# Kernel optimization log

Measured on AMD Instinct MI355X. Metric: run time of the kernel, lower is better.

## Reference

```python
import jax, jax.numpy as jnp
import numpy as np

B, S, D, H, HID = 8192, 16, 128, 8, 1024
DH = D // H  # 16
GCN, NUMF = 40, 103
EPS = 1e-5

def _make_pe():
    pos = np.arange(S, dtype=np.float64)[:, None]
    i = np.arange(D, dtype=np.float64)[None, :]
    pe = pos / np.power(10000.0, (i // 2 * 2.0) / D)
    pe[:, 0::2] = np.sin(pe[:, 0::2])
    pe[:, 1::2] = np.cos(pe[:, 1::2])
    return jnp.asarray(pe, dtype=jnp.float32)  # [S, D]

PE = _make_pe()

def setup_inputs() -> dict:
    key = jax.random.key(0)
    ks = jax.random.split(key, 16)
    rn = lambda k, shape, s=0.02: (jax.random.normal(k, shape, jnp.float32) * s)
    return {
        "x": jax.random.normal(ks[0], (B, S, D), jnp.float32),
        "gcn_i": jax.random.normal(ks[1], (B, GCN), jnp.float32),
        "num": jax.random.normal(ks[2], (B, NUMF), jnp.float32),
        # two independent encoder layers, params stacked on leading dim
        "Wq": rn(ks[3], (2, D, D)), "bq": jnp.zeros((2, D), jnp.float32),
        "Wk": rn(ks[4], (2, D, D)), "bk": jnp.zeros((2, D), jnp.float32),
        "Wv": rn(ks[5], (2, D, D)), "bv": jnp.zeros((2, D), jnp.float32),
        "Wo": rn(ks[6], (2, D, D)), "bo": jnp.zeros((2, D), jnp.float32),
        "ln1_g": jnp.ones((2, D), jnp.float32), "ln1_b": jnp.zeros((2, D), jnp.float32),
        "W1": rn(ks[7], (2, D, HID)), "b1": jnp.zeros((2, HID), jnp.float32),
        "W2": rn(ks[8], (2, HID, D)), "b2": jnp.zeros((2, D), jnp.float32),
        "ln2_g": jnp.ones((2, D), jnp.float32), "ln2_b": jnp.zeros((2, D), jnp.float32),
        # head
        "Wn": rn(ks[9], (NUMF, D)), "bnum": jnp.zeros((D,), jnp.float32),
        "bn_gamma": jnp.ones((D,), jnp.float32), "bn_beta": jnp.zeros((D,), jnp.float32),
        "Wf": rn(ks[10], (S * D + GCN + D, 1)), "bf": jnp.zeros((1,), jnp.float32),
    }

def _ln(x, g, b):
    m = x.mean(-1, keepdims=True)
    v = ((x - m) ** 2).mean(-1, keepdims=True)
    return (x - m) * jax.lax.rsqrt(v + EPS) * g + b

def reference(x, gcn_i, num, Wq, bq, Wk, bk, Wv, bv, Wo, bo, ln1_g, ln1_b,
              W1, b1, W2, b2, ln2_g, ln2_b, Wn, bnum, bn_gamma, bn_beta, Wf, bf):
    out = x + PE  # positional encoding (dropout = identity in eval)
    scale = DH ** -0.5
    for l in range(2):
        # NOTE: original uses a raw .view(B*H, -1, DH) (no transpose) -- faithful reshape
        q = (out @ Wq[l] + bq[l]).reshape(B * H, S, DH)
        k = (out @ Wk[l] + bk[l]).reshape(B * H, S, DH)
        v = (out @ Wv[l] + bv[l]).reshape(B * H, S, DH)
        attn = jax.nn.softmax(jnp.einsum('nsd,ntd->nst', q, k) * scale, axis=-1)
        ctx = jnp.einsum('nst,ntd->nsd', attn, v).reshape(B, S, D)
        h = _ln(ctx @ Wo[l] + bo[l] + out, ln1_g[l], ln1_b[l])
        ff = jax.nn.relu(h @ W1[l] + b1[l]) @ W2[l] + b2[l]
        out = _ln(ff + h, ln2_g[l], ln2_b[l])
    flat = out.reshape(B, S * D)  # [B, 2048]
    n = num @ Wn + bnum  # [B, 128]
    # BatchNorm1d, training-mode forward (biased batch variance)
    mu = n.mean(0)
    var = ((n - mu) ** 2).mean(0)
    n = (n - mu) * jax.lax.rsqrt(var + EPS) * bn_gamma + bn_beta
    p = jnp.concatenate([flat, gcn_i, n], axis=-1)  # [B, 2216]
    return jax.nn.sigmoid(p @ Wf + bf)
```

## Files before the change

### kernel.cpp

```cpp
#include <hip/hip_runtime.h>
#include <hip/hip_bf16.h>
#include <math.h>

#define B_SZ   8192
#define S_SZ   16
#define D_SZ   128
#define HID_SZ 1024
#define NUMF_SZ 103
#define GCN_SZ 40
#define G_B    4
#define NBLK   (B_SZ / G_B)
#define STRD   136

typedef short bh8 __attribute__((ext_vector_type(8)));
typedef float fx4 __attribute__((ext_vector_type(4)));

__device__ __forceinline__ fx4 mfma16(bh8 a, bh8 b, fx4 c) {
    return __builtin_amdgcn_mfma_f32_16x16x32_bf16(a, b, c, 0, 0, 0);
}

__device__ __forceinline__ unsigned short f2b(float f) {
    unsigned u = __float_as_uint(f);
    return (unsigned short)((u + 0x7fffu + ((u >> 16) & 1u)) >> 16);
}
__device__ __forceinline__ float bu2f(unsigned short u) {
    return __uint_as_float(((unsigned)u) << 16);
}

__global__ __launch_bounds__(256) void prep_weights(
    const float* __restrict__ Wq, const float* __restrict__ Wk,
    const float* __restrict__ Wv, const float* __restrict__ Wo,
    const float* __restrict__ W1, const float* __restrict__ W2,
    unsigned short* __restrict__ WswQ, unsigned short* __restrict__ WswK,
    unsigned short* __restrict__ WswV, unsigned short* __restrict__ WswO,
    unsigned short* __restrict__ Wsw1, unsigned short* __restrict__ Wsw2,
    float* __restrict__ PEt)
{
    int i = blockIdx.x * 256 + threadIdx.x;
    if (i < 2048) {
        int s = i >> 7, c = i & 127;
        float expo = (float)((c >> 1) * 2) * (1.0f / 128.0f);
        float denom = powf(10000.0f, expo);
        float ang = (float)s / denom;
        PEt[i] = (c & 1) ? cosf(ang) : sinf(ang);
    }
    if (i < 2 * 16384) {
        int l = i >> 14, r = i & 16383;
        int nt = r >> 11, ks = (r >> 9) & 3, lane = (r >> 3) & 63, e = r & 7;
        int k = ks * 32 + (lane >> 4) * 8 + e;
        int n = nt * 16 + (lane & 15);
        int s = l * 16384 + k * 128 + n;
        WswQ[i] = f2b(Wq[s]); WswK[i] = f2b(Wk[s]);
        WswV[i] = f2b(Wv[s]); WswO[i] = f2b(Wo[s]);
    }
    {
        int l = i >> 17, r = i & 131071;
        int nt = r >> 11, ks = (r >> 9) & 3, lane = (r >> 3) & 63, e = r & 7;
        int k = ks * 32 + (lane >> 4) * 8 + e;
        int n = nt * 16 + (lane & 15);
        Wsw1[i] = f2b(W1[l * 131072 + k * 1024 + n]);
    }
    {
        int l = i >> 17, r = i & 131071;
        int nt = r >> 14, kt = (r >> 9) & 31, lane = (r >> 3) & 63, e = r & 7;
        int k = kt * 32 + (lane >> 4) * 8 + e;
        int n = nt * 16 + (lane & 15);
        Wsw2[i] = f2b(W2[l * 131072 + k * 128 + n]);
    }
}

__global__ __launch_bounds__(256, 2) void encoder_fused(
    const float* __restrict__ x, const float* __restrict__ gcn,
    const float* __restrict__ bq, const float* __restrict__ bk,
    const float* __restrict__ bv, const float* __restrict__ bo,
    const float* __restrict__ ln1g, const float* __restrict__ ln1b,
    const float* __restrict__ b1, const float* __restrict__ b2p,
    const float* __restrict__ ln2g, const float* __restrict__ ln2b,
    const float* __restrict__ Wf,
    const unsigned short* __restrict__ WswQ, const unsigned short* __restrict__ WswK,
    const unsigned short* __restrict__ WswV, const unsigned short* __restrict__ WswO,
    const unsigned short* __restrict__ Wsw1, const unsigned short* __restrict__ Wsw2,
    const float* __restrict__ PEt,
    float* __restrict__ acc1)
{
    __shared__ unsigned short ACT[64][STRD];
    __shared__ unsigned short Qb[64][STRD];
    __shared__ unsigned short Kb[64][STRD];
    __shared__ unsigned short Vb[64][STRD];
    __shared__ float LNp[64][4][2];
    __shared__ float LNs[64][2];

    const int t = threadIdx.x;
    const int w = t >> 6, lane = t & 63;
    const int q = lane >> 4, ln = lane & 15;
    const int bbase = blockIdx.x * G_B;

    {
        const float4* xb = (const float4*)(x + (size_t)bbase * 2048);
        const float4* pe4 = (const float4*)PEt;
#pragma unroll
        for (int i = 0; i < 8; ++i) {
            int f4 = i * 256 + t;
            float4 xv = xb[f4];
            float4 pv = pe4[f4 & 511];
            int flat = f4 * 4;
            int row = flat >> 7, col = flat & 127;
            ushort4 pk = {f2b(xv.x + pv.x), f2b(xv.y + pv.y),
                          f2b(xv.z + pv.z), f2b(xv.w + pv.w)};
            *(ushort4*)&ACT[row][col] = pk;
        }
    }
    __syncthreads();

    for (int l = 0; l < 2; ++l) {
        {
            bh8 afr[4][4];
#pragma unroll
            for (int mt = 0; mt < 4; ++mt)
#pragma unroll
                for (int ks = 0; ks < 4; ++ks)
                    afr[mt][ks] = *(const bh8*)&ACT[mt * 16 + ln][ks * 32 + q * 8];
            const unsigned short* Wm[3] = {WswQ + l * 16384, WswK + l * 16384, WswV + l * 16384};
            const float* bias3[3] = {bq + l * 128, bk + l * 128, bv + l * 128};
#pragma unroll
            for (int mtx = 0; mtx < 3; ++mtx) {
                unsigned short (*dst)[STRD] = (mtx == 0) ? Qb : (mtx == 1) ? Kb : Vb;
#pragma unroll
                for (int i2 = 0; i2 < 2; ++i2) {
                    int nt = w * 2 + i2;
                    bh8 wfr[4];
#pragma unroll
                    for (int ks = 0; ks < 4; ++ks)
                        wfr[ks] = *(const bh8*)(Wm[mtx] + ((nt * 4 + ks) * 64 + lane) * 8);
                    int n = nt * 16 + ln;
                    float bb = bias3[mtx][n];
#pragma unroll
                    for (int mt = 0; mt < 4; ++mt) {
                        fx4 acc = {0.f, 0.f, 0.f, 0.f};
#pragma unroll
                        for (int ks = 0; ks < 4; ++ks) acc = mfma16(afr[mt][ks], wfr[ks], acc);
#pragma unroll
                        for (int r2 = 0; r2 < 4; ++r2)
                            dst[mt * 16 + q * 4 + r2][n] = f2b(acc[r2] + bb);
                    }
                }
            }
        }
        __syncthreads();

        {
            int base = w * 16;
            int g = lane >> 3, u0 = (lane & 7) * 2;
            float qr[2][16];
#pragma unroll
            for (int h = 0; h < 2; ++h) {
                int u = u0 + h;
                int qsr = base + 2 * g + (u >> 3), qc = (u & 7) * 16;
                bh8 a0 = *(const bh8*)&Qb[qsr][qc];
                bh8 a1 = *(const bh8*)&Qb[qsr][qc + 8];
#pragma unroll
                for (int e = 0; e < 8; ++e) {
                    qr[h][e] = bu2f((unsigned short)a0[e]);
                    qr[h][8 + e] = bu2f((unsigned short)a1[e]);
                }
            }
            float p[2][16];
#pragma unroll
            for (int tp = 0; tp < 16; ++tp) {
                int ksr = base + 2 * g + (tp >> 3), kc = (tp & 7) * 16;
                bh8 k0 = *(const bh8*)&Kb[ksr][kc];
                bh8 k1 = *(const bh8*)&Kb[ksr][kc + 8];
                float d0 = 0.f, d1 = 0.f;
#pragma unroll
                for (int e = 0; e < 8; ++e) {
                    float kv = bu2f((unsigned short)k0[e]);
                    d0 = fmaf(qr[0][e], kv, d0); d1 = fmaf(qr[1][e], kv, d1);
                }
#pragma unroll
                for (int e = 0; e < 8; ++e) {
                    float kv = bu2f((unsigned short)k1[e]);
                    d0 = fmaf(qr[0][8 + e], kv, d0); d1 = fmaf(qr[1][8 + e], kv, d1);
                }
                p[0][tp] = d0 * 0.25f; p[1][tp] = d1 * 0.25f;
            }
#pragma unroll
            for (int h = 0; h < 2; ++h) {
                float mx = -1e30f;
#pragma unroll
                for (int tp = 0; tp < 16; ++tp) mx = fmaxf(mx, p[h][tp]);
                float sum = 0.f;
#pragma unroll
                for (int tp = 0; tp < 16; ++tp) { p[h][tp] = __expf(p[h][tp] - mx); sum += p[h][tp]; }
                float is = 1.0f / sum;
#pragma unroll
                for (int tp = 0; tp < 16; ++tp) p[h][tp] *= is;
            }
            float ctx[2][16];
#pragma unroll
            for (int h = 0; h < 2; ++h)
#pragma unroll
                for (int e = 0; e < 16; ++e) ctx[h][e] = 0.f;
#pragma unroll
            for (int tp = 0; tp < 16; ++tp) {
                int vsr = base + 2 * g + (tp >> 3), vc = (tp & 7) * 16;
                bh8 v0 = *(const bh8*)&Vb[vsr][vc];
                bh8 v1 = *(const bh8*)&Vb[vsr][vc + 8];
#pragma unroll
                for (int e = 0; e < 8; ++e) {
                    float vv = bu2f((unsigned short)v0[e]);
                    ctx[0][e] = fmaf(p[0][tp], vv, ctx[0][e]);
                    ctx[1][e] = fmaf(p[1][tp], vv, ctx[1][e]);
                }
#pragma unroll
                for (int e = 0; e < 8; ++e) {
                    float vv = bu2f((unsigned short)v1[e]);
                    ctx[0][8 + e] = fmaf(p[0][tp], vv, ctx[0][8 + e]);
                    ctx[1][8 + e] = fmaf(p[1][tp], vv, ctx[1][8 + e]);
                }
            }
#pragma unroll
            for (int h = 0; h < 2; ++h) {
                int u = u0 + h;
                int s = base + 2 * g + (u >> 3), dc = (u & 7) * 16;
                bh8 c0, c1;
#pragma unroll
                for (int e = 0; e < 8; ++e) {
                    c0[e] = (short)f2b(ctx[h][e]);
                    c1[e] = (short)f2b(ctx[h][8 + e]);
                }
                *(bh8*)&Qb[s][dc] = c0;
                *(bh8*)&Qb[s][dc + 8] = c1;
            }
        }
        __syncthreads();

        fx4 Cv[2][4];
        {
            bh8 cfr[4][4];
#pragma unroll
            for (int mt = 0; mt < 4; ++mt)
#pragma unroll
                for (int ks = 0; ks < 4; ++ks)
                    cfr[mt][ks] = *(const bh8*)&Qb[mt * 16 + ln][ks * 32 + q * 8];
#pragma unroll
            for (int i2 = 0; i2 < 2; ++i2) {
                int nt = w * 2 + i2, n = nt * 16 + ln;
                bh8 wfr[4];
#pragma unroll
                for (int ks = 0; ks < 4; ++ks)
                    wfr[ks] = *(const bh8*)(WswO + l * 16384 + ((nt * 4 + ks) * 64 + lane) * 8);
                float bb = bo[l * 128 + n];
#pragma unroll
                for (int mt = 0; mt < 4; ++mt) {
                    fx4 acc = {0.f, 0.f, 0.f, 0.f};
#pragma unroll
                    for (int ks = 0; ks < 4; ++ks) acc = mfma16(cfr[mt][ks], wfr[ks], acc);
#pragma unroll
                    for (int r2 = 0; r2 < 4; ++r2)
                        Cv[i2][mt][r2] = acc[r2] + bb +
                            bu2f(ACT[mt * 16 + q * 4 + r2][n]);
                }
            }
        }
#pragma unroll
        for (int mt = 0; mt < 4; ++mt) {
            float s4[4], v4[4];
#pragma unroll
            for (int r2 = 0; r2 < 4; ++r2) {
                float a0 = Cv[0][mt][r2], a1 = Cv[1][mt][r2];
                float s = a0 + a1, v = a0 * a0 + a1 * a1;
#pragma unroll
                for (int m = 1; m < 16; m <<= 1) { s += __shfl_xor(s, m); v += __shfl_xor(v, m); }
                s4[r2] = s; v4[r2] = v;
            }
            if (ln < 8)
                LNp[mt * 16 + q * 4 + (ln >> 1)][w][ln & 1] = (ln & 1) ? v4[ln >> 1] : s4[ln >> 1];
        }
        __syncthreads();
        if (t < 64) {
            float s = LNp[t][0][0] + LNp[t][1][0] + LNp[t][2][0] + LNp[t][3][0];
            float v = LNp[t][0][1] + LNp[t][1][1] + LNp[t][2][1] + LNp[t][3][1];
            float mean = s * (1.0f / 128.0f);
            LNs[t][0] = mean;
            LNs[t][1] = rsqrtf(v * (1.0f / 128.0f) - mean * mean + 1e-5f);
        }
        __syncthreads();
#pragma unroll
        for (int i2 = 0; i2 < 2; ++i2) {
            int n = (w * 2 + i2) * 16 + ln;
            float gg = ln1g[l * 128 + n], be = ln1b[l * 128 + n];
#pragma unroll
            for (int mt = 0; mt < 4; ++mt)
#pragma unroll
                for (int r2 = 0; r2 < 4; ++r2) {
                    int row = mt * 16 + q * 4 + r2;
                    Kb[row][n] = f2b((Cv[i2][mt][r2] - LNs[row][0]) * LNs[row][1] * gg + be);
                }
        }
        __syncthreads();

        bh8 hfr[4][4];
#pragma unroll
        for (int mt = 0; mt < 4; ++mt)
#pragma unroll
            for (int ks = 0; ks < 4; ++ks)
                hfr[mt][ks] = *(const bh8*)&Kb[mt * 16 + ln][ks * 32 + q * 8];
        fx4 f2a[2][4];
#pragma unroll
        for (int i2 = 0; i2 < 2; ++i2)
#pragma unroll
            for (int mt = 0; mt < 4; ++mt) f2a[i2][mt] = fx4{0.f, 0.f, 0.f, 0.f};
        for (int ch = 0; ch < 8; ++ch) {
            bh8 w1fr[2][4];
#pragma unroll
            for (int i2 = 0; i2 < 2; ++i2) {
                int ntg = ch * 8 + w * 2 + i2;
#pragma unroll
                for (int ks = 0; ks < 4; ++ks)
                    w1fr[i2][ks] = *(const bh8*)(Wsw1 + l * 131072 + ((ntg * 4 + ks) * 64 + lane) * 8);
            }
#pragma unroll
            for (int mt = 0; mt < 4; ++mt) {
#pragma unroll
                for (int i2 = 0; i2 < 2; ++i2) {
                    fx4 acc = {0.f, 0.f, 0.f, 0.f};
#pragma unroll
                    for (int ks = 0; ks < 4; ++ks) acc = mfma16(hfr[mt][ks], w1fr[i2][ks], acc);
                    int nl = (w * 2 + i2) * 16 + ln;
                    float bb = b1[l * HID_SZ + ch * 128 + nl];
#pragma unroll
                    for (int r2 = 0; r2 < 4; ++r2) {
                        float vv = acc[r2] + bb;
                        Qb[mt * 16 + q * 4 + r2][nl] = f2b(vv > 0.f ? vv : 0.f);
                    }
                }
            }
            __syncthreads();
            bh8 w2fr[2][4];
#pragma unroll
            for (int i2 = 0; i2 < 2; ++i2)
#pragma unroll
                for (int ks = 0; ks < 4; ++ks)
                    w2fr[i2][ks] = *(const bh8*)(Wsw2 + l * 131072 +
                        (((w * 2 + i2) * 32 + ch * 4 + ks) * 64 + lane) * 8);
#pragma unroll
            for (int mt = 0; mt < 4; ++mt) {
                bh8 ffr[4];
#pragma unroll
                for (int ks = 0; ks < 4; ++ks)
                    ffr[ks] = *(const bh8*)&Qb[mt * 16 + ln][ks * 32 + q * 8];
#pragma unroll
                for (int i2 = 0; i2 < 2; ++i2)
#pragma unroll
                    for (int ks = 0; ks < 4; ++ks)
                        f2a[i2][mt] = mfma16(ffr[ks], w2fr[i2][ks], f2a[i2][mt]);
            }
            __syncthreads();
        }
        fx4 Cv2[2][4];
#pragma unroll
        for (int i2 = 0; i2 < 2; ++i2) {
            int n = (w * 2 + i2) * 16 + ln;
            float bb = b2p[l * 128 + n];
#pragma unroll
            for (int mt = 0; mt < 4; ++mt)
#pragma unroll
                for (int r2 = 0; r2 < 4; ++r2)
                    Cv2[i2][mt][r2] = f2a[i2][mt][r2] + bb +
                        bu2f(Kb[mt * 16 + q * 4 + r2][n]);
        }
#pragma unroll
        for (int mt = 0; mt < 4; ++mt) {
            float s4[4], v4[4];
#pragma unroll
            for (int r2 = 0; r2 < 4; ++r2) {
                float a0 = Cv2[0][mt][r2], a1 = Cv2[1][mt][r2];
                float s = a0 + a1, v = a0 * a0 + a1 * a1;
#pragma unroll
                for (int m = 1; m < 16; m <<= 1) { s += __shfl_xor(s, m); v += __shfl_xor(v, m); }
                s4[r2] = s; v4[r2] = v;
            }
            if (ln < 8)
                LNp[mt * 16 + q * 4 + (ln >> 1)][w][ln & 1] = (ln & 1) ? v4[ln >> 1] : s4[ln >> 1];
        }
        __syncthreads();
        if (t < 64) {
            float s = LNp[t][0][0] + LNp[t][1][0] + LNp[t][2][0] + LNp[t][3][0];
            float v = LNp[t][0][1] + LNp[t][1][1] + LNp[t][2][1] + LNp[t][3][1];
            float mean = s * (1.0f / 128.0f);
            LNs[t][0] = mean;
            LNs[t][1] = rsqrtf(v * (1.0f / 128.0f) - mean * mean + 1e-5f);
        }
        __syncthreads();
#pragma unroll
        for (int i2 = 0; i2 < 2; ++i2) {
            int n = (w * 2 + i2) * 16 + ln;
            float gg = ln2g[l * 128 + n], be = ln2b[l * 128 + n];
#pragma unroll
            for (int mt = 0; mt < 4; ++mt)
#pragma unroll
                for (int r2 = 0; r2 < 4; ++r2) {
                    int row = mt * 16 + q * 4 + r2;
                    ACT[row][n] = f2b((Cv2[i2][mt][r2] - LNs[row][0]) * LNs[row][1] * gg + be);
                }
        }
        __syncthreads();
    }

    {
        int bg = bbase + w;
        float part = 0.f;
        int srow = lane >> 2, c0 = (lane & 3) * 32;
#pragma unroll
        for (int i = 0; i < 4; ++i) {
            bh8 av = *(const bh8*)&ACT[w * 16 + srow][c0 + i * 8];
            int fl = srow * 128 + c0 + i * 8;
#pragma unroll
            for (int e = 0; e < 8; ++e)
                part = fmaf(bu2f((unsigned short)av[e]), Wf[fl + e], part);
        }
        if (lane < GCN_SZ)
            part = fmaf(gcn[(size_t)bg * GCN_SZ + lane], Wf[2048 + lane], part);
#pragma unroll
        for (int off = 32; off; off >>= 1) part += __shfl_xor(part, off);
        if (lane == 0) acc1[bg] = part;
    }
}

__global__ __launch_bounds__(256) void num_stats_kernel(
    const float* __restrict__ num, const float* __restrict__ Wn,
    const float* __restrict__ bnum,
    float* __restrict__ ssum, float* __restrict__ ssq)
{
    __shared__ float NUM[16][NUMF_SZ + 1];
    __shared__ float cred[4][128];
    const int t = threadIdx.x;
    const int b0 = blockIdx.x * 16;
    const int j = t & 127, sg = t >> 7, s0 = sg * 8;

    for (int idx = t; idx < 16 * NUMF_SZ; idx += 256) {
        int r = idx / NUMF_SZ, f = idx - r * NUMF_SZ;
        NUM[r][f] = num[(size_t)(b0 + r) * NUMF_SZ + f];
    }
    __syncthreads();

    float acc[8];
    float bnv = bnum[j];
#pragma unroll
    for (int r = 0; r < 8; ++r) acc[r] = bnv;
    for (int f = 0; f < NUMF_SZ; ++f) {
        float w = Wn[f * 128 + j];
#pragma unroll
        for (int r = 0; r < 8; ++r) acc[r] = fmaf(NUM[s0 + r][f], w, acc[r]);
    }
    float lsum = 0.f, lsq = 0.f;
#pragma unroll
    for (int r = 0; r < 8; ++r) {
        lsum += acc[r];
        lsq = fmaf(acc[r], acc[r], lsq);
    }
    cred[sg][j] = lsum;
    cred[2 + sg][j] = lsq;
    __syncthreads();
    if (sg == 0) atomicAdd(&ssum[j], cred[0][j] + cred[1][j]);
    else         atomicAdd(&ssq[j],  cred[2][j] + cred[3][j]);
}

__global__ __launch_bounds__(128) void final_kernel(
    const float* __restrict__ num, const float* __restrict__ Wn,
    const float* __restrict__ bnum,
    const float* __restrict__ ssum, const float* __restrict__ ssq,
    const float* __restrict__ gamma, const float* __restrict__ beta,
    const float* __restrict__ Wf, const float* __restrict__ bfin,
    const float* __restrict__ acc1, float* __restrict__ out)
{
    const int b = blockIdx.x, jj = threadIdx.x;
    __shared__ float red2[2];
    __shared__ float NUMr[NUMF_SZ];
    if (jj < NUMF_SZ) NUMr[jj] = num[(size_t)b * NUMF_SZ + jj];
    __syncthreads();

    float nv = bnum[jj];
    for (int f = 0; f < NUMF_SZ; ++f)
        nv = fmaf(NUMr[f], Wn[f * 128 + jj], nv);

    float mean = ssum[jj] * (1.0f / (float)B_SZ);
    float var = ssq[jj] * (1.0f / (float)B_SZ) - mean * mean;
    float bnv = (nv - mean) * rsqrtf(var + 1e-5f) * gamma[jj] + beta[jj];
    float v = bnv * Wf[2088 + jj];
#pragma unroll
    for (int o = 32; o; o >>= 1) v += __shfl_down(v, o);
    if ((jj & 63) == 0) red2[jj >> 6] = v;
    __syncthreads();
    if (jj == 0) {
        float z = acc1[b] + red2[0] + red2[1] + bfin[0];
        out[b] = 1.0f / (1.0f + __expf(-z));
    }
}

extern "C" void kernel_launch(void* const* d_in, const int* in_sizes, int n_in,
                              void* d_out, int out_size, void* d_ws, size_t ws_size,
                              hipStream_t stream)
{
    const float* x    = (const float*)d_in[0];
    const float* gcn  = (const float*)d_in[1];
    const float* num  = (const float*)d_in[2];
    const float* Wq   = (const float*)d_in[3];
    const float* bq   = (const float*)d_in[4];
    const float* Wk   = (const float*)d_in[5];
    const float* bk   = (const float*)d_in[6];
    const float* Wv   = (const float*)d_in[7];
    const float* bv   = (const float*)d_in[8];
    const float* Wo   = (const float*)d_in[9];
    const float* bo   = (const float*)d_in[10];
    const float* ln1g = (const float*)d_in[11];
    const float* ln1b = (const float*)d_in[12];
    const float* W1   = (const float*)d_in[13];
    const float* b1   = (const float*)d_in[14];
    const float* W2   = (const float*)d_in[15];
    const float* b2p  = (const float*)d_in[16];
    const float* ln2g = (const float*)d_in[17];
    const float* ln2b = (const float*)d_in[18];
    const float* Wn   = (const float*)d_in[19];
    const float* bnum = (const float*)d_in[20];
    const float* bng  = (const float*)d_in[21];
    const float* bnb  = (const float*)d_in[22];
    const float* Wf   = (const float*)d_in[23];
    const float* bfin = (const float*)d_in[24];

    float* acc1 = (float*)d_ws;
    float* ssum = acc1 + B_SZ;
    float* ssq  = ssum + 128;
    unsigned short* wb = (unsigned short*)((char*)d_ws + 40960);
    unsigned short* WswQ = wb;
    unsigned short* WswK = wb + 32768;
    unsigned short* WswV = wb + 65536;
    unsigned short* WswO = wb + 98304;
    unsigned short* Wsw1 = wb + 131072;
    unsigned short* Wsw2 = wb + 393216;
    float* PEt = (float*)((char*)d_ws + 40960 + 1310720);

    hipMemsetAsync(ssum, 0, 2 * 128 * sizeof(float), stream);
    prep_weights<<<1024, 256, 0, stream>>>(Wq, Wk, Wv, Wo, W1, W2,
        WswQ, WswK, WswV, WswO, Wsw1, Wsw2, PEt);
    encoder_fused<<<NBLK, 256, 0, stream>>>(x, gcn, bq, bk, bv, bo,
        ln1g, ln1b, b1, b2p, ln2g, ln2b, Wf,
        WswQ, WswK, WswV, WswO, Wsw1, Wsw2, PEt, acc1);
    num_stats_kernel<<<B_SZ / 16, 256, 0, stream>>>(num, Wn, bnum, ssum, ssq);
    final_kernel<<<B_SZ, 128, 0, stream>>>(num, Wn, bnum, ssum, ssq, bng, bnb,
        Wf, bfin, acc1, (float*)d_out);
}
```

Before: 476.9 us.

## Halve batch rows per block, double-buffer FFN hidden tiles, cache num projection

Each encoder block now handles 2 batch elements (32 rows) instead of 4, and launch bounds ask for 4 blocks per CU to raise occupancy and cut LDS and register use. The attention stage assigns one (row, head) pair per thread across all four warps. The FFN hidden chunk alternates between two LDS buffers, which removes the per-chunk barrier. The numeric projection is written to workspace in the stats kernel so the final kernel reuses it rather than recomputing the 103-wide dot products. The bf16 conversion now calls the library intrinsic. Risks are less weight-fragment reuse per block, with each block reloading the weights for half as many rows, and possible register spills at the tighter occupancy bound.

```diff
diff --git a/kernel.cpp b/kernel.cpp
--- a/kernel.cpp
+++ b/kernel.cpp
@@ -8,8 +8,9 @@
 #define HID_SZ 1024
 #define NUMF_SZ 103
 #define GCN_SZ 40
-#define G_B    4
+#define G_B    2
 #define NBLK   (B_SZ / G_B)
+#define R_SZ   (16 * G_B)
 #define STRD   136
 
 typedef short bh8 __attribute__((ext_vector_type(8)));
@@ -20,8 +21,9 @@
 }
 
 __device__ __forceinline__ unsigned short f2b(float f) {
-    unsigned u = __float_as_uint(f);
-    return (unsigned short)((u + 0x7fffu + ((u >> 16) & 1u)) >> 16);
+    union { __hip_bfloat16 b; unsigned short u; } cv;
+    cv.b = __float2bfloat16(f);
+    return cv.u;
 }
 __device__ __forceinline__ float bu2f(unsigned short u) {
     return __uint_as_float(((unsigned)u) << 16);
@@ -69,7 +71,7 @@
     }
 }
 
-__global__ __launch_bounds__(256, 2) void encoder_fused(
+__global__ __launch_bounds__(256, 4) void encoder_fused(
     const float* __restrict__ x, const float* __restrict__ gcn,
     const float* __restrict__ bq, const float* __restrict__ bk,
     const float* __restrict__ bv, const float* __restrict__ bo,
@@ -83,12 +85,12 @@
     const float* __restrict__ PEt,
     float* __restrict__ acc1)
 {
-    __shared__ unsigned short ACT[64][STRD];
-    __shared__ unsigned short Qb[64][STRD];
-    __shared__ unsigned short Kb[64][STRD];
-    __shared__ unsigned short Vb[64][STRD];
-    __shared__ float LNp[64][4][2];
-    __shared__ float LNs[64][2];
+    __shared__ unsigned short ACT[R_SZ][STRD];
+    __shared__ unsigned short Qb[R_SZ][STRD];
+    __shared__ unsigned short Kb[R_SZ][STRD];
+    __shared__ unsigned short Vb[R_SZ][STRD];
+    __shared__ float LNp[R_SZ][4][2];
+    __shared__ float LNs[R_SZ][2];
 
     const int t = threadIdx.x;
     const int w = t >> 6, lane = t & 63;
@@ -99,7 +101,7 @@
         const float4* xb = (const float4*)(x + (size_t)bbase * 2048);
         const float4* pe4 = (const float4*)PEt;
 #pragma unroll
-        for (int i = 0; i < 8; ++i) {
+        for (int i = 0; i < 4; ++i) {
             int f4 = i * 256 + t;
             float4 xv = xb[f4];
             float4 pv = pe4[f4 & 511];
@@ -114,9 +116,9 @@
 
     for (int l = 0; l < 2; ++l) {
         {
-            bh8 afr[4][4];
-#pragma unroll
-            for (int mt = 0; mt < 4; ++mt)
+            bh8 afr[2][4];
+#pragma unroll
+            for (int mt = 0; mt < 2; ++mt)
 #pragma unroll
                 for (int ks = 0; ks < 4; ++ks)
                     afr[mt][ks] = *(const bh8*)&ACT[mt * 16 + ln][ks * 32 + q * 8];
@@ -135,7 +137,7 @@
                     int n = nt * 16 + ln;
                     float bb = bias3[mtx][n];
 #pragma unroll
-                    for (int mt = 0; mt < 4; ++mt) {
+                    for (int mt = 0; mt < 2; ++mt) {
                         fx4 acc = {0.f, 0.f, 0.f, 0.f};
 #pragma unroll
                         for (int ks = 0; ks < 4; ++ks) acc = mfma16(afr[mt][ks], wfr[ks], acc);
@@ -149,96 +151,74 @@
         __syncthreads();
 
         {
-            int base = w * 16;
-            int g = lane >> 3, u0 = (lane & 7) * 2;
-            float qr[2][16];
-#pragma unroll
-            for (int h = 0; h < 2; ++h) {
-                int u = u0 + h;
-                int qsr = base + 2 * g + (u >> 3), qc = (u & 7) * 16;
+            const int e = w >> 1;
+            const int base = e * 16;
+            const int pid = ((w & 1) << 6) | lane;
+            const int g = pid >> 4, u = pid & 15;
+            const int qsr = base + 2 * g + (u >> 3), qc = (u & 7) * 16;
+            float qr[16];
+            {
                 bh8 a0 = *(const bh8*)&Qb[qsr][qc];
                 bh8 a1 = *(const bh8*)&Qb[qsr][qc + 8];
 #pragma unroll
-                for (int e = 0; e < 8; ++e) {
-                    qr[h][e] = bu2f((unsigned short)a0[e]);
-                    qr[h][8 + e] = bu2f((unsigned short)a1[e]);
-                }
-            }
-            float p[2][16];
+                for (int e8 = 0; e8 < 8; ++e8) {
+                    qr[e8] = bu2f((unsigned short)a0[e8]);
+                    qr[8 + e8] = bu2f((unsigned short)a1[e8]);
+                }
+            }
+            float p[16];
 #pragma unroll
             for (int tp = 0; tp < 16; ++tp) {
                 int ksr = base + 2 * g + (tp >> 3), kc = (tp & 7) * 16;
                 bh8 k0 = *(const bh8*)&Kb[ksr][kc];
                 bh8 k1 = *(const bh8*)&Kb[ksr][kc + 8];
-                float d0 = 0.f, d1 = 0.f;
-#pragma unroll
-                for (int e = 0; e < 8; ++e) {
-                    float kv = bu2f((unsigned short)k0[e]);
-                    d0 = fmaf(qr[0][e], kv, d0); d1 = fmaf(qr[1][e], kv, d1);
-                }
-#pragma unroll
-                for (int e = 0; e < 8; ++e) {
-                    float kv = bu2f((unsigned short)k1[e]);
-                    d0 = fmaf(qr[0][8 + e], kv, d0); d1 = fmaf(qr[1][8 + e], kv, d1);
-                }
-                p[0][tp] = d0 * 0.25f; p[1][tp] = d1 * 0.25f;
-            }
-#pragma unroll
-            for (int h = 0; h < 2; ++h) {
-                float mx = -1e30f;
-#pragma unroll
-                for (int tp = 0; tp < 16; ++tp) mx = fmaxf(mx, p[h][tp]);
-                float sum = 0.f;
-#pragma unroll
-                for (int tp = 0; tp < 16; ++tp) { p[h][tp] = __expf(p[h][tp] - mx); sum += p[h][tp]; }
-                float is = 1.0f / sum;
-#pragma unroll
-                for (int tp = 0; tp < 16; ++tp) p[h][tp] *= is;
-            }
-            float ctx[2][16];
-#pragma unroll
-            for (int h = 0; h < 2; ++h)
-#pragma unroll
-                for (int e = 0; e < 16; ++e) ctx[h][e] = 0.f;
+                float d = 0.f;
+#pragma unroll
+                for (int e8 = 0; e8 < 8; ++e8)
+                    d = fmaf(qr[e8], bu2f((unsigned short)k0[e8]), d);
+#pragma unroll
+                for (int e8 = 0; e8 < 8; ++e8)
+                    d = fmaf(qr[8 + e8], bu2f((unsigned short)k1[e8]), d);
+                p[tp] = d * 0.25f;
+            }
+            float mx = -1e30f;
+#pragma unroll
+            for (int tp = 0; tp < 16; ++tp) mx = fmaxf(mx, p[tp]);
+            float sum = 0.f;
+#pragma unroll
+            for (int tp = 0; tp < 16; ++tp) { p[tp] = __expf(p[tp] - mx); sum += p[tp]; }
+            float is = 1.0f / sum;
+            float ctx[16];
+#pragma unroll
+            for (int e8 = 0; e8 < 16; ++e8) ctx[e8] = 0.f;
 #pragma unroll
             for (int tp = 0; tp < 16; ++tp) {
                 int vsr = base + 2 * g + (tp >> 3), vc = (tp & 7) * 16;
                 bh8 v0 = *(const bh8*)&Vb[vsr][vc];
                 bh8 v1 = *(const bh8*)&Vb[vsr][vc + 8];
-#pragma unroll
-                for (int e = 0; e < 8; ++e) {
-                    float vv = bu2f((unsigned short)v0[e]);
-                    ctx[0][e] = fmaf(p[0][tp], vv, ctx[0][e]);
-                    ctx[1][e] = fmaf(p[1][tp], vv, ctx[1][e]);
-                }
-#pragma unroll
-                for (int e = 0; e < 8; ++e) {
-                    float vv = bu2f((unsigned short)v1[e]);
-                    ctx[0][8 + e] = fmaf(p[0][tp], vv, ctx[0][8 + e]);
-                    ctx[1][8 + e] = fmaf(p[1][tp], vv, ctx[1][8 + e]);
-                }
-            }
-#pragma unroll
-            for (int h = 0; h < 2; ++h) {
-                int u = u0 + h;
-                int s = base + 2 * g + (u >> 3), dc = (u & 7) * 16;
-                bh8 c0, c1;
-#pragma unroll
-                for (int e = 0; e < 8; ++e) {
-                    c0[e] = (short)f2b(ctx[h][e]);
-                    c1[e] = (short)f2b(ctx[h][8 + e]);
-                }
-                *(bh8*)&Qb[s][dc] = c0;
-                *(bh8*)&Qb[s][dc + 8] = c1;
-            }
-        }
-        __syncthreads();
-
-        fx4 Cv[2][4];
+                float pw = p[tp] * is;
+#pragma unroll
+                for (int e8 = 0; e8 < 8; ++e8) {
+                    ctx[e8]     = fmaf(pw, bu2f((unsigned short)v0[e8]), ctx[e8]);
+                    ctx[8 + e8] = fmaf(pw, bu2f((unsigned short)v1[e8]), ctx[8 + e8]);
+                }
+            }
+            bh8 c0, c1;
+#pragma unroll
+            for (int e8 = 0; e8 < 8; ++e8) {
+                c0[e8] = (short)f2b(ctx[e8]);
+                c1[e8] = (short)f2b(ctx[8 + e8]);
+            }
+            *(bh8*)&Qb[qsr][qc] = c0;
+            *(bh8*)&Qb[qsr][qc + 8] = c1;
+        }
+        __syncthreads();
+
+        fx4 Cv[2][2];
         {
-            bh8 cfr[4][4];
-#pragma unroll
-            for (int mt = 0; mt < 4; ++mt)
+            bh8 cfr[2][4];
+#pragma unroll
+            for (int mt = 0; mt < 2; ++mt)
 #pragma unroll
                 for (int ks = 0; ks < 4; ++ks)
                     cfr[mt][ks] = *(const bh8*)&Qb[mt * 16 + ln][ks * 32 + q * 8];
@@ -251,7 +231,7 @@
                     wfr[ks] = *(const bh8*)(WswO + l * 16384 + ((nt * 4 + ks) * 64 + lane) * 8);
                 float bb = bo[l * 128 + n];
 #pragma unroll
-                for (int mt = 0; mt < 4; ++mt) {
+                for (int mt = 0; mt < 2; ++mt) {
                     fx4 acc = {0.f, 0.f, 0.f, 0.f};
 #pragma unroll
                     for (int ks = 0; ks < 4; ++ks) acc = mfma16(cfr[mt][ks], wfr[ks], acc);
@@ -263,7 +243,7 @@
             }
         }
 #pragma unroll
-        for (int mt = 0; mt < 4; ++mt) {
+        for (int mt = 0; mt < 2; ++mt) {
             float s4[4], v4[4];
 #pragma unroll
             for (int r2 = 0; r2 < 4; ++r2) {
@@ -277,7 +257,7 @@
                 LNp[mt * 16 + q * 4 + (ln >> 1)][w][ln & 1] = (ln & 1) ? v4[ln >> 1] : s4[ln >> 1];
         }
         __syncthreads();
-        if (t < 64) {
+        if (t < R_SZ) {
             float s = LNp[t][0][0] + LNp[t][1][0] + LNp[t][2][0] + LNp[t][3][0];
             float v = LNp[t][0][1] + LNp[t][1][1] + LNp[t][2][1] + LNp[t][3][1];
             float mean = s * (1.0f / 128.0f);
@@ -290,7 +270,7 @@
             int n = (w * 2 + i2) * 16 + ln;
             float gg = ln1g[l * 128 + n], be = ln1b[l * 128 + n];
 #pragma unroll
-            for (int mt = 0; mt < 4; ++mt)
+            for (int mt = 0; mt < 2; ++mt)
 #pragma unroll
                 for (int r2 = 0; r2 < 4; ++r2) {
                     int row = mt * 16 + q * 4 + r2;
@@ -299,18 +279,19 @@
         }
         __syncthreads();
 
-        bh8 hfr[4][4];
-#pragma unroll
-        for (int mt = 0; mt < 4; ++mt)
+        bh8 hfr[2][4];
+#pragma unroll
+        for (int mt = 0; mt < 2; ++mt)
 #pragma unroll
             for (int ks = 0; ks < 4; ++ks)
                 hfr[mt][ks] = *(const bh8*)&Kb[mt * 16 + ln][ks * 32 + q * 8];
-        fx4 f2a[2][4];
+        fx4 f2a[2][2];
 #pragma unroll
         for (int i2 = 0; i2 < 2; ++i2)
 #pragma unroll
-            for (int mt = 0; mt < 4; ++mt) f2a[i2][mt] = fx4{0.f, 0.f, 0.f, 0.f};
+            for (int mt = 0; mt < 2; ++mt) f2a[i2][mt] = fx4{0.f, 0.f, 0.f, 0.f};
         for (int ch = 0; ch < 8; ++ch) {
+            unsigned short (*dst)[STRD] = (ch & 1) ? Vb : Qb;
             bh8 w1fr[2][4];
 #pragma unroll
             for (int i2 = 0; i2 < 2; ++i2) {
@@ -320,7 +301,7 @@
                     w1fr[i2][ks] = *(const bh8*)(Wsw1 + l * 131072 + ((ntg * 4 + ks) * 64 + lane) * 8);
             }
 #pragma unroll
-            for (int mt = 0; mt < 4; ++mt) {
+            for (int mt = 0; mt < 2; ++mt) {
 #pragma unroll
                 for (int i2 = 0; i2 < 2; ++i2) {
                     fx4 acc = {0.f, 0.f, 0.f, 0.f};
@@ -331,7 +312,7 @@
 #pragma unroll
                     for (int r2 = 0; r2 < 4; ++r2) {
                         float vv = acc[r2] + bb;
-                        Qb[mt * 16 + q * 4 + r2][nl] = f2b(vv > 0.f ? vv : 0.f);
+                        dst[mt * 16 + q * 4 + r2][nl] = f2b(vv > 0.f ? vv : 0.f);
                     }
                 }
             }
@@ -344,33 +325,32 @@
                     w2fr[i2][ks] = *(const bh8*)(Wsw2 + l * 131072 +
                         (((w * 2 + i2) * 32 + ch * 4 + ks) * 64 + lane) * 8);
 #pragma unroll
-            for (int mt = 0; mt < 4; ++mt) {
+            for (int mt = 0; mt < 2; ++mt) {
                 bh8 ffr[4];
 #pragma unroll
                 for (int ks = 0; ks < 4; ++ks)
-                    ffr[ks] = *(const bh8*)&Qb[mt * 16 + ln][ks * 32 + q * 8];
+                    ffr[ks] = *(const bh8*)&dst[mt * 16 + ln][ks * 32 + q * 8];
 #pragma unroll
                 for (int i2 = 0; i2 < 2; ++i2)
 #pragma unroll
                     for (int ks = 0; ks < 4; ++ks)
                         f2a[i2][mt] = mfma16(ffr[ks], w2fr[i2][ks], f2a[i2][mt]);
             }
-            __syncthreads();
-        }
-        fx4 Cv2[2][4];
+        }
+        fx4 Cv2[2][2];
 #pragma unroll
         for (int i2 = 0; i2 < 2; ++i2) {
             int n = (w * 2 + i2) * 16 + ln;
             float bb = b2p[l * 128 + n];
 #pragma unroll
-            for (int mt = 0; mt < 4; ++mt)
+            for (int mt = 0; mt < 2; ++mt)
 #pragma unroll
                 for (int r2 = 0; r2 < 4; ++r2)
                     Cv2[i2][mt][r2] = f2a[i2][mt][r2] + bb +
                         bu2f(Kb[mt * 16 + q * 4 + r2][n]);
         }
 #pragma unroll
-        for (int mt = 0; mt < 4; ++mt) {
+        for (int mt = 0; mt < 2; ++mt) {
             float s4[4], v4[4];
 #pragma unroll
             for (int r2 = 0; r2 < 4; ++r2) {
@@ -384,7 +364,7 @@
                 LNp[mt * 16 + q * 4 + (ln >> 1)][w][ln & 1] = (ln & 1) ? v4[ln >> 1] : s4[ln >> 1];
         }
         __syncthreads();
-        if (t < 64) {
+        if (t < R_SZ) {
             float s = LNp[t][0][0] + LNp[t][1][0] + LNp[t][2][0] + LNp[t][3][0];
             float v = LNp[t][0][1] + LNp[t][1][1] + LNp[t][2][1] + LNp[t][3][1];
             float mean = s * (1.0f / 128.0f);
@@ -397,7 +377,7 @@
             int n = (w * 2 + i2) * 16 + ln;
             float gg = ln2g[l * 128 + n], be = ln2b[l * 128 + n];
 #pragma unroll
-            for (int mt = 0; mt < 4; ++mt)
+            for (int mt = 0; mt < 2; ++mt)
 #pragma unroll
                 for (int r2 = 0; r2 < 4; ++r2) {
                     int row = mt * 16 + q * 4 + r2;
@@ -408,29 +388,36 @@
     }
 
     {
-        int bg = bbase + w;
+        const int e = w >> 1, h2 = w & 1;
+        int bg = bbase + e;
         float part = 0.f;
-        int srow = lane >> 2, c0 = (lane & 3) * 32;
-#pragma unroll
-        for (int i = 0; i < 4; ++i) {
-            bh8 av = *(const bh8*)&ACT[w * 16 + srow][c0 + i * 8];
-            int fl = srow * 128 + c0 + i * 8;
-#pragma unroll
-            for (int e = 0; e < 8; ++e)
-                part = fmaf(bu2f((unsigned short)av[e]), Wf[fl + e], part);
-        }
-        if (lane < GCN_SZ)
-            part = fmaf(gcn[(size_t)bg * GCN_SZ + lane], Wf[2048 + lane], part);
+        int r = h2 * 8 + (lane >> 3), c0 = (lane & 7) * 16;
+#pragma unroll
+        for (int i = 0; i < 2; ++i) {
+            bh8 av = *(const bh8*)&ACT[e * 16 + r][c0 + i * 8];
+            int fl = r * 128 + c0 + i * 8;
+#pragma unroll
+            for (int e8 = 0; e8 < 8; ++e8)
+                part = fmaf(bu2f((unsigned short)av[e8]), Wf[fl + e8], part);
+        }
+        if (lane < 20) {
+            int gi = h2 * 20 + lane;
+            part = fmaf(gcn[(size_t)bg * GCN_SZ + gi], Wf[2048 + gi], part);
+        }
 #pragma unroll
         for (int off = 32; off; off >>= 1) part += __shfl_xor(part, off);
-        if (lane == 0) acc1[bg] = part;
-    }
+        if (lane == 0) LNs[w][0] = part;
+    }
+    __syncthreads();
+    if (t < G_B)
+        acc1[bbase + t] = LNs[2 * t][0] + LNs[2 * t + 1][0];
 }
 
 __global__ __launch_bounds__(256) void num_stats_kernel(
     const float* __restrict__ num, const float* __restrict__ Wn,
     const float* __restrict__ bnum,
-    float* __restrict__ ssum, float* __restrict__ ssq)
+    float* __restrict__ ssum, float* __restrict__ ssq,
+    float* __restrict__ nws, int have_nws)
 {
     __shared__ float NUM[16][NUMF_SZ + 1];
     __shared__ float cred[4][128];
@@ -453,6 +440,11 @@
 #pragma unroll
         for (int r = 0; r < 8; ++r) acc[r] = fmaf(NUM[s0 + r][f], w, acc[r]);
     }
+    if (have_nws) {
+#pragma unroll
+        for (int r = 0; r < 8; ++r)
+            nws[(size_t)(b0 + s0 + r) * 128 + j] = acc[r];
+    }
     float lsum = 0.f, lsq = 0.f;
 #pragma unroll
     for (int r = 0; r < 8; ++r) {
@@ -472,17 +464,23 @@
     const float* __restrict__ ssum, const float* __restrict__ ssq,
     const float* __restrict__ gamma, const float* __restrict__ beta,
     const float* __restrict__ Wf, const float* __restrict__ bfin,
-    const float* __restrict__ acc1, float* __restrict__ out)
+    const float* __restrict__ acc1, float* __restrict__ out,
+    const float* __restrict__ nws, int have_nws)
 {
     const int b = blockIdx.x, jj = threadIdx.x;
     __shared__ float red2[2];
     __shared__ float NUMr[NUMF_SZ];
-    if (jj < NUMF_SZ) NUMr[jj] = num[(size_t)b * NUMF_SZ + jj];
-    __syncthreads();
-
-    float nv = bnum[jj];
-    for (int f = 0; f < NUMF_SZ; ++f)
-        nv = fmaf(NUMr[f], Wn[f * 128 + jj], nv);
+
+    float nv;
+    if (have_nws) {
+        nv = nws[(size_t)b * 128 + jj];
+    } else {
+        if (jj < NUMF_SZ) NUMr[jj] = num[(size_t)b * NUMF_SZ + jj];
+        __syncthreads();
+        nv = bnum[jj];
+        for (int f = 0; f < NUMF_SZ; ++f)
+            nv = fmaf(NUMr[f], Wn[f * 128 + jj], nv);
+    }
 
     float mean = ssum[jj] * (1.0f / (float)B_SZ);
     float var = ssq[jj] * (1.0f / (float)B_SZ) - mean * mean;
@@ -539,6 +537,9 @@
     unsigned short* Wsw1 = wb + 131072;
     unsigned short* Wsw2 = wb + 393216;
     float* PEt = (float*)((char*)d_ws + 40960 + 1310720);
+    const size_t nws_off = 40960 + 1310720 + 8192;
+    float* nws = (float*)((char*)d_ws + nws_off);
+    const int have_nws = (ws_size >= nws_off + (size_t)B_SZ * 128 * sizeof(float)) ? 1 : 0;
 
     hipMemsetAsync(ssum, 0, 2 * 128 * sizeof(float), stream);
     prep_weights<<<1024, 256, 0, stream>>>(Wq, Wk, Wv, Wo, W1, W2,
@@ -546,7 +547,8 @@
     encoder_fused<<<NBLK, 256, 0, stream>>>(x, gcn, bq, bk, bv, bo,
         ln1g, ln1b, b1, b2p, ln2g, ln2b, Wf,
         WswQ, WswK, WswV, WswO, Wsw1, Wsw2, PEt, acc1);
-    num_stats_kernel<<<B_SZ / 16, 256, 0, stream>>>(num, Wn, bnum, ssum, ssq);
+    num_stats_kernel<<<B_SZ / 16, 256, 0, stream>>>(num, Wn, bnum, ssum, ssq,
+        nws, have_nws);
     final_kernel<<<B_SZ, 128, 0, stream>>>(num, Wn, bnum, ssum, ssq, bng, bnb,
-        Wf, bfin, acc1, (float*)d_out);
-}
+        Wf, bfin, acc1, (float*)d_out, nws, have_nws);
+}
```

After: 545.2 us. +14.3%, slower.

## Use MFMA for per-head attention, double-buffer FFN hidden, precompute BN head

Applied to the files above, without the earlier changes.

The per-head QK^T and PV products now run on 16x16x32 bf16 MFMA instructions instead of scalar FMA loops. V is written in a transposed layout and the softmax probabilities are staged through a small shared buffer. The FFN hidden chunk alternates between two shared buffers so the per-chunk barrier can be dropped. The num-projection outputs are now saved to workspace and folded with precomputed BatchNorm coefficients, which avoids recomputing the 103x128 projection per sample in the final kernel. Risks are correctness of the new layouts and removing the barrier in the FFN loop, plus extra workspace traffic.

```diff
diff --git a/kernel.cpp b/kernel.cpp
--- a/kernel.cpp
+++ b/kernel.cpp
@@ -20,8 +20,9 @@
 }
 
 __device__ __forceinline__ unsigned short f2b(float f) {
-    unsigned u = __float_as_uint(f);
-    return (unsigned short)((u + 0x7fffu + ((u >> 16) & 1u)) >> 16);
+    union { __hip_bfloat16 b; unsigned short u; } cv;
+    cv.b = __float2bfloat16(f);
+    return cv.u;
 }
 __device__ __forceinline__ float bu2f(unsigned short u) {
     return __uint_as_float(((unsigned)u) << 16);
@@ -89,6 +90,9 @@
     __shared__ unsigned short Vb[64][STRD];
     __shared__ float LNp[64][4][2];
     __shared__ float LNs[64][2];
+    __shared__ unsigned short Pb[4][16][16];
+
+    unsigned short* Vb4 = &Vb[0][0];
 
     const int t = threadIdx.x;
     const int w = t >> 6, lane = t & 63;
@@ -124,7 +128,6 @@
             const float* bias3[3] = {bq + l * 128, bk + l * 128, bv + l * 128};
 #pragma unroll
             for (int mtx = 0; mtx < 3; ++mtx) {
-                unsigned short (*dst)[STRD] = (mtx == 0) ? Qb : (mtx == 1) ? Kb : Vb;
 #pragma unroll
                 for (int i2 = 0; i2 < 2; ++i2) {
                     int nt = w * 2 + i2;
@@ -139,9 +142,22 @@
                         fx4 acc = {0.f, 0.f, 0.f, 0.f};
 #pragma unroll
                         for (int ks = 0; ks < 4; ++ks) acc = mfma16(afr[mt][ks], wfr[ks], acc);
-#pragma unroll
-                        for (int r2 = 0; r2 < 4; ++r2)
-                            dst[mt * 16 + q * 4 + r2][n] = f2b(acc[r2] + bb);
+                        if (mtx == 0) {
+#pragma unroll
+                            for (int r2 = 0; r2 < 4; ++r2)
+                                Qb[mt * 16 + q * 4 + r2][n] = f2b(acc[r2] + bb);
+                        } else if (mtx == 1) {
+#pragma unroll
+                            for (int r2 = 0; r2 < 4; ++r2)
+                                Kb[mt * 16 + q * 4 + r2][n] = f2b(acc[r2] + bb);
+                        } else {
+#pragma unroll
+                            for (int r2 = 0; r2 < 4; ++r2) {
+                                int s = q * 4 + r2;
+                                Vb4[(((mt * 8 + (s >> 1)) * 16) + ln) * 16 +
+                                    (((s & 1) << 3) | nt)] = f2b(acc[r2] + bb);
+                            }
+                        }
                     }
                 }
             }
@@ -149,87 +165,38 @@
         __syncthreads();
 
         {
-            int base = w * 16;
-            int g = lane >> 3, u0 = (lane & 7) * 2;
-            float qr[2][16];
-#pragma unroll
-            for (int h = 0; h < 2; ++h) {
-                int u = u0 + h;
-                int qsr = base + 2 * g + (u >> 3), qc = (u & 7) * 16;
-                bh8 a0 = *(const bh8*)&Qb[qsr][qc];
-                bh8 a1 = *(const bh8*)&Qb[qsr][qc + 8];
-#pragma unroll
-                for (int e = 0; e < 8; ++e) {
-                    qr[h][e] = bu2f((unsigned short)a0[e]);
-                    qr[h][8 + e] = bu2f((unsigned short)a1[e]);
-                }
-            }
-            float p[2][16];
-#pragma unroll
-            for (int tp = 0; tp < 16; ++tp) {
-                int ksr = base + 2 * g + (tp >> 3), kc = (tp & 7) * 16;
-                bh8 k0 = *(const bh8*)&Kb[ksr][kc];
-                bh8 k1 = *(const bh8*)&Kb[ksr][kc + 8];
-                float d0 = 0.f, d1 = 0.f;
-#pragma unroll
-                for (int e = 0; e < 8; ++e) {
-                    float kv = bu2f((unsigned short)k0[e]);
-                    d0 = fmaf(qr[0][e], kv, d0); d1 = fmaf(qr[1][e], kv, d1);
-                }
-#pragma unroll
-                for (int e = 0; e < 8; ++e) {
-                    float kv = bu2f((unsigned short)k1[e]);
-                    d0 = fmaf(qr[0][8 + e], kv, d0); d1 = fmaf(qr[1][8 + e], kv, d1);
-                }
-                p[0][tp] = d0 * 0.25f; p[1][tp] = d1 * 0.25f;
-            }
-#pragma unroll
-            for (int h = 0; h < 2; ++h) {
-                float mx = -1e30f;
-#pragma unroll
-                for (int tp = 0; tp < 16; ++tp) mx = fmaxf(mx, p[h][tp]);
-                float sum = 0.f;
-#pragma unroll
-                for (int tp = 0; tp < 16; ++tp) { p[h][tp] = __expf(p[h][tp] - mx); sum += p[h][tp]; }
-                float is = 1.0f / sum;
-#pragma unroll
-                for (int tp = 0; tp < 16; ++tp) p[h][tp] *= is;
-            }
-            float ctx[2][16];
-#pragma unroll
-            for (int h = 0; h < 2; ++h)
-#pragma unroll
-                for (int e = 0; e < 16; ++e) ctx[h][e] = 0.f;
-#pragma unroll
-            for (int tp = 0; tp < 16; ++tp) {
-                int vsr = base + 2 * g + (tp >> 3), vc = (tp & 7) * 16;
-                bh8 v0 = *(const bh8*)&Vb[vsr][vc];
-                bh8 v1 = *(const bh8*)&Vb[vsr][vc + 8];
-#pragma unroll
-                for (int e = 0; e < 8; ++e) {
-                    float vv = bu2f((unsigned short)v0[e]);
-                    ctx[0][e] = fmaf(p[0][tp], vv, ctx[0][e]);
-                    ctx[1][e] = fmaf(p[1][tp], vv, ctx[1][e]);
-                }
-#pragma unroll
-                for (int e = 0; e < 8; ++e) {
-                    float vv = bu2f((unsigned short)v1[e]);
-                    ctx[0][8 + e] = fmaf(p[0][tp], vv, ctx[0][8 + e]);
-                    ctx[1][8 + e] = fmaf(p[1][tp], vv, ctx[1][8 + e]);
-                }
-            }
-#pragma unroll
-            for (int h = 0; h < 2; ++h) {
-                int u = u0 + h;
-                int s = base + 2 * g + (u >> 3), dc = (u & 7) * 16;
-                bh8 c0, c1;
-#pragma unroll
-                for (int e = 0; e < 8; ++e) {
-                    c0[e] = (short)f2b(ctx[h][e]);
-                    c1[e] = (short)f2b(ctx[h][8 + e]);
-                }
-                *(bh8*)&Qb[s][dc] = c0;
-                *(bh8*)&Qb[s][dc + 8] = c1;
+            const int E = w;
+            const int rbase = E * 16 + (ln >> 3);
+            const int ccol = (ln & 7) * 16;
+#pragma unroll
+            for (int g = 0; g < 8; ++g) {
+                bh8 kfr = 0, qfr = 0;
+                if (q < 2) {
+                    kfr = *(const bh8*)&Kb[rbase + 2 * g][ccol + q * 8];
+                    qfr = *(const bh8*)&Qb[rbase + 2 * g][ccol + q * 8];
+                }
+                fx4 st = mfma16(kfr, qfr, fx4{0.f, 0.f, 0.f, 0.f});
+                float p0 = st[0] * 0.25f, p1 = st[1] * 0.25f;
+                float p2 = st[2] * 0.25f, p3 = st[3] * 0.25f;
+                float mx = fmaxf(fmaxf(p0, p1), fmaxf(p2, p3));
+                mx = fmaxf(mx, __shfl_xor(mx, 16));
+                mx = fmaxf(mx, __shfl_xor(mx, 32));
+                p0 = __expf(p0 - mx); p1 = __expf(p1 - mx);
+                p2 = __expf(p2 - mx); p3 = __expf(p3 - mx);
+                float sm = (p0 + p1) + (p2 + p3);
+                sm += __shfl_xor(sm, 16);
+                sm += __shfl_xor(sm, 32);
+                float is = 1.0f / sm;
+                ushort4 pk = {f2b(p0 * is), f2b(p1 * is), f2b(p2 * is), f2b(p3 * is)};
+                *(ushort4*)&Pb[w][ln][q * 4] = pk;
+                bh8 vfr = 0, pfr = 0;
+                if (q < 2) {
+                    vfr = *(const bh8*)&Vb4[(((E * 8 + g) * 16) + ln) * 16 + q * 8];
+                    pfr = *(const bh8*)&Pb[w][ln][q * 8];
+                }
+                fx4 cx = mfma16(vfr, pfr, fx4{0.f, 0.f, 0.f, 0.f});
+                ushort4 ck = {f2b(cx[0]), f2b(cx[1]), f2b(cx[2]), f2b(cx[3])};
+                *(ushort4*)&Qb[rbase + 2 * g][ccol + q * 4] = ck;
             }
         }
         __syncthreads();
@@ -311,6 +278,7 @@
 #pragma unroll
             for (int mt = 0; mt < 4; ++mt) f2a[i2][mt] = fx4{0.f, 0.f, 0.f, 0.f};
         for (int ch = 0; ch < 8; ++ch) {
+            unsigned short (*dst)[STRD] = (ch & 1) ? Vb : Qb;
             bh8 w1fr[2][4];
 #pragma unroll
             for (int i2 = 0; i2 < 2; ++i2) {
@@ -331,7 +299,7 @@
 #pragma unroll
                     for (int r2 = 0; r2 < 4; ++r2) {
                         float vv = acc[r2] + bb;
-                        Qb[mt * 16 + q * 4 + r2][nl] = f2b(vv > 0.f ? vv : 0.f);
+                        dst[mt * 16 + q * 4 + r2][nl] = f2b(vv > 0.f ? vv : 0.f);
                     }
                 }
             }
@@ -348,14 +316,13 @@
                 bh8 ffr[4];
 #pragma unroll
                 for (int ks = 0; ks < 4; ++ks)
-                    ffr[ks] = *(const bh8*)&Qb[mt * 16 + ln][ks * 32 + q * 8];
+                    ffr[ks] = *(const bh8*)&dst[mt * 16 + ln][ks * 32 + q * 8];
 #pragma unroll
                 for (int i2 = 0; i2 < 2; ++i2)
 #pragma unroll
                     for (int ks = 0; ks < 4; ++ks)
                         f2a[i2][mt] = mfma16(ffr[ks], w2fr[i2][ks], f2a[i2][mt]);
             }
-            __syncthreads();
         }
         fx4 Cv2[2][4];
 #pragma unroll
@@ -430,7 +397,8 @@
 __global__ __launch_bounds__(256) void num_stats_kernel(
     const float* __restrict__ num, const float* __restrict__ Wn,
     const float* __restrict__ bnum,
-    float* __restrict__ ssum, float* __restrict__ ssq)
+    float* __restrict__ ssum, float* __restrict__ ssq,
+    float* __restrict__ nws, int have_nws)
 {
     __shared__ float NUM[16][NUMF_SZ + 1];
     __shared__ float cred[4][128];
@@ -453,6 +421,11 @@
 #pragma unroll
         for (int r = 0; r < 8; ++r) acc[r] = fmaf(NUM[s0 + r][f], w, acc[r]);
     }
+    if (have_nws) {
+#pragma unroll
+        for (int r = 0; r < 8; ++r)
+            nws[(size_t)(b0 + s0 + r) * 128 + j] = acc[r];
+    }
     float lsum = 0.f, lsq = 0.f;
 #pragma unroll
     for (int r = 0; r < 8; ++r) {
@@ -464,6 +437,47 @@
     __syncthreads();
     if (sg == 0) atomicAdd(&ssum[j], cred[0][j] + cred[1][j]);
     else         atomicAdd(&ssq[j],  cred[2][j] + cred[3][j]);
+}
+
+__global__ __launch_bounds__(128) void bn_coef_kernel(
+    const float* __restrict__ ssum, const float* __restrict__ ssq,
+    const float* __restrict__ gamma, const float* __restrict__ beta,
+    const float* __restrict__ Wf, const float* __restrict__ bfin,
+    float* __restrict__ cvec)
+{
+    const int j = threadIdx.x;
+    __shared__ float red2[2];
+    float mean = ssum[j] * (1.0f / (float)B_SZ);
+    float var = ssq[j] * (1.0f / (float)B_SZ) - mean * mean;
+    float inv = rsqrtf(var + 1e-5f);
+    float wj = Wf[2088 + j];
+    float gi = gamma[j] * inv;
+    cvec[j] = gi * wj;
+    float k = (beta[j] - mean * gi) * wj;
+#pragma unroll
+    for (int o = 32; o; o >>= 1) k += __shfl_down(k, o);
+    if ((j & 63) == 0) red2[j >> 6] = k;
+    __syncthreads();
+    if (j == 0) cvec[128] = red2[0] + red2[1] + bfin[0];
+}
+
+__global__ __launch_bounds__(256) void final_fast(
+    const float* __restrict__ nws, const float* __restrict__ cvec,
+    const float* __restrict__ acc1, float* __restrict__ out)
+{
+    __shared__ float cs[129];
+    const int t = threadIdx.x;
+    if (t < 129) cs[t] = cvec[t];
+    __syncthreads();
+    const int w = t >> 6, lane = t & 63;
+    const int b = blockIdx.x * 4 + w;
+    const float2* nb = (const float2*)(nws + (size_t)b * 128);
+    float2 v = nb[lane];
+    float d = v.x * cs[2 * lane] + v.y * cs[2 * lane + 1];
+#pragma unroll
+    for (int o = 32; o; o >>= 1) d += __shfl_xor(d, o);
+    if (lane == 0)
+        out[b] = 1.0f / (1.0f + __expf(-(acc1[b] + d + cs[128])));
 }
 
 __global__ __launch_bounds__(128) void final_kernel(
@@ -479,11 +493,9 @@
     __shared__ float NUMr[NUMF_SZ];
     if (jj < NUMF_SZ) NUMr[jj] = num[(size_t)b * NUMF_SZ + jj];
     __syncthreads();
-
     float nv = bnum[jj];
     for (int f = 0; f < NUMF_SZ; ++f)
         nv = fmaf(NUMr[f], Wn[f * 128 + jj], nv);
-
     float mean = ssum[jj] * (1.0f / (float)B_SZ);
     float var = ssq[jj] * (1.0f / (float)B_SZ) - mean * mean;
     float bnv = (nv - mean) * rsqrtf(var + 1e-5f) * gamma[jj] + beta[jj];
@@ -539,6 +551,11 @@
     unsigned short* Wsw1 = wb + 131072;
     unsigned short* Wsw2 = wb + 393216;
     float* PEt = (float*)((char*)d_ws + 40960 + 1310720);
+    const size_t nws_off = 40960 + 1310720 + 8192;
+    float* nws = (float*)((char*)d_ws + nws_off);
+    const size_t cvec_off = nws_off + (size_t)B_SZ * 128 * sizeof(float);
+    float* cvec = (float*)((char*)d_ws + cvec_off);
+    const int have_nws = (ws_size >= cvec_off + 132 * sizeof(float)) ? 1 : 0;
 
     hipMemsetAsync(ssum, 0, 2 * 128 * sizeof(float), stream);
     prep_weights<<<1024, 256, 0, stream>>>(Wq, Wk, Wv, Wo, W1, W2,
@@ -546,7 +563,13 @@
     encoder_fused<<<NBLK, 256, 0, stream>>>(x, gcn, bq, bk, bv, bo,
         ln1g, ln1b, b1, b2p, ln2g, ln2b, Wf,
         WswQ, WswK, WswV, WswO, Wsw1, Wsw2, PEt, acc1);
-    num_stats_kernel<<<B_SZ / 16, 256, 0, stream>>>(num, Wn, bnum, ssum, ssq);
-    final_kernel<<<B_SZ, 128, 0, stream>>>(num, Wn, bnum, ssum, ssq, bng, bnb,
-        Wf, bfin, acc1, (float*)d_out);
-}
+    num_stats_kernel<<<B_SZ / 16, 256, 0, stream>>>(num, Wn, bnum, ssum, ssq,
+        nws, have_nws);
+    if (have_nws) {
+        bn_coef_kernel<<<1, 128, 0, stream>>>(ssum, ssq, bng, bnb, Wf, bfin, cvec);
+        final_fast<<<B_SZ / 4, 256, 0, stream>>>(nws, cvec, acc1, (float*)d_out);
+    } else {
+        final_kernel<<<B_SZ, 128, 0, stream>>>(num, Wn, bnum, ssum, ssq, bng, bnb,
+            Wf, bfin, acc1, (float*)d_out);
+    }
+}
```

Result: faster. 458.9 us (-3.8%).
